# Kernel tuning notes

Hardware: AMD Instinct MI355X
Metric: run time of the kernel (lower is better)

## Reference

```python
import jax, jax.numpy as jnp
import numpy as np

B, S, D = 16, 2048, 128
SCALE = 1.0 / float(np.sqrt(D))  # scale = 1/sqrt(dim_K) per docstring


def setup_inputs() -> dict:
    key = jax.random.key(0)
    kq, kk, kv = jax.random.split(key, 3)
    Q = jax.random.normal(kq, (B, S, D), dtype=jnp.float32)
    K = jax.random.normal(kk, (B, S, D), dtype=jnp.float32)
    V = jax.random.normal(kv, (B, S, D), dtype=jnp.float32)
    return {"Q": Q, "K": K, "V": V}


def reference(Q, K, V):
    # attention = Q @ K^T * scale  -> [B, S, S]
    attn = jnp.einsum('bqd,bkd->bqk', Q, K) * SCALE
    attn = jax.nn.softmax(attn, axis=-1)
    # context = attn @ V -> [B, S, D]
    context = jnp.einsum('bqk,bkd->bqd', attn, V)
    return context
```

## Files before the change

kernel.cpp:

```cpp
#include <hip/hip_runtime.h>
#include <hip/hip_bf16.h>


#define NB 16
#define NS 2048
#define ND 128
#define KVB 32
#define NTT (NS / KVB)
#define IMG 16384
#define QSC (0.08838834764831845f * 1.4426950408889634f)

typedef __attribute__((ext_vector_type(8))) short bf16x8;
typedef __attribute__((ext_vector_type(4))) short short4v;
typedef __attribute__((ext_vector_type(16))) float f32x16;
typedef __attribute__((ext_vector_type(4))) int int4v;

__device__ __forceinline__ short f2bf(float f) {
    unsigned u = __builtin_bit_cast(unsigned, f);
    return (short)((u + 0x7fffu + ((u >> 16) & 1u)) >> 16);
}

#if __has_builtin(__builtin_amdgcn_exp2f)
#define EXP2F(x) __builtin_amdgcn_exp2f(x)
#else
#define EXP2F(x) __expf((x) * 0.6931471805599453f)
#endif

__device__ __forceinline__ void gll16(const void* g, void* l) {
    __builtin_amdgcn_global_load_lds(
        (const __attribute__((address_space(1))) uint32_t*)g,
        (__attribute__((address_space(3))) uint32_t*)l, 16, 0, 0);
}

__global__ __launch_bounds__(256, 2)
void prep_kv(const float* __restrict__ Kg, const float* __restrict__ Vg,
             uint8_t* __restrict__ ws) {
    __shared__ __align__(16) uint8_t img[2 * IMG];
    const int tid = threadIdx.x;
    const int t = blockIdx.x, b = blockIdx.y;
    const float* Kb = Kg + ((size_t)b * NS + (size_t)t * 64) * ND;
    const float* Vb = Vg + ((size_t)b * NS + (size_t)t * 64) * ND;
#pragma unroll
    for (int it = 0; it < 8; ++it) {
        int idx = it * 256 + tid;
        int r  = idx >> 5;
        int c4 = (idx & 31) << 2;
        int sub = (r >> 5) * (2 * 8192);
        int rr = r & 31;
        float4 kvv = *(const float4*)(Kb + (size_t)r * ND + c4);
        short4v ks = { f2bf(kvv.x), f2bf(kvv.y), f2bf(kvv.z), f2bf(kvv.w) };
        *(short4v*)&img[sub + rr * 256 + ((c4 * 2) ^ ((rr & 7) << 4))] = ks;
        float4 vv = *(const float4*)(Vb + (size_t)r * ND + c4);
        float vf[4] = { vv.x, vv.y, vv.z, vv.w };
#pragma unroll
        for (int di = 0; di < 4; ++di) {
            int d = c4 + di;
            *(short*)&img[sub + 8192 + d * 64 + ((rr * 2) ^ (((d >> 1) & 3) << 4))]
                = f2bf(vf[di]);
        }
    }
    __syncthreads();
    float4* dst = (float4*)(ws + (size_t)(b * (NTT / 2) + t) * (2 * IMG));
    const float4* srcl = (const float4*)img;
#pragma unroll
    for (int j = 0; j < 8; ++j)
        dst[j * 256 + tid] = srcl[j * 256 + tid];
}

__global__ __launch_bounds__(768, 3)
void sdpa_fwd(const float* __restrict__ Qg, const uint8_t* __restrict__ ws,
              float* __restrict__ Og) {
    __shared__ __align__(16) uint8_t kv[3][3][IMG];

    const int tid  = threadIdx.x;
    const int w    = tid >> 6;
    const int wq   = w & 3;
    const int wh   = w >> 2;
    const int lane = tid & 63;
    const int lr_  = lane & 31;
    const int hi   = lane >> 5;

    const int tlo  = (wh == 0) ? 0 : (22 + 21 * (wh - 1));
    const int tcnt = (wh == 0) ? 22 : 21;

    const int gid  = blockIdx.x;
    const int b    = (gid & 7) * 2 + ((gid >> 3) & 1);
    const int qblk = gid >> 4;
    const int q0w  = qblk * 128 + wq * 32;

    bf16x8 qf[8];
    {
        const float* qrow = Qg + ((size_t)b * NS + q0w + lr_) * ND;
#pragma unroll
        for (int dc = 0; dc < 8; ++dc) {
            const float4* p = (const float4*)(qrow + dc * 16 + hi * 8);
            float4 x0 = p[0], x1 = p[1];
            bf16x8 f;
            f[0] = f2bf(x0.x * QSC); f[1] = f2bf(x0.y * QSC);
            f[2] = f2bf(x0.z * QSC); f[3] = f2bf(x0.w * QSC);
            f[4] = f2bf(x1.x * QSC); f[5] = f2bf(x1.y * QSC);
            f[6] = f2bf(x1.z * QSC); f[7] = f2bf(x1.w * QSC);
            qf[dc] = f;
        }
    }

    f32x16 acc[4];
#pragma unroll
    for (int n = 0; n < 4; ++n)
#pragma unroll
        for (int r = 0; r < 16; ++r) acc[n][r] = 0.f;
    float m_run = -__builtin_inff();
    float l_run = 0.f;

    const uint8_t* wsb = ws + (size_t)b * NTT * IMG;

    const int kbase = lr_ * 256 + ((hi * 16) ^ ((lr_ & 7) << 4));
    const int vbase = 8192 + lr_ * 64 + ((hi * 16) ^ (((lr_ >> 1) & 3) << 4));

    auto st = [&](int tt, uint8_t* dst) {
        if (tt < tcnt) {
            const uint8_t* src = wsb + (size_t)(tlo + tt) * IMG
                                     + (size_t)(wq * 4096 + lane * 16);
            gll16(src,        dst);
            gll16(src + 1024, dst + 1024);
            gll16(src + 2048, dst + 2048);
            gll16(src + 3072, dst + 3072);
        }
    };

    auto qk = [&](int p, const uint8_t* img_, f32x16& sN) {
        if (p < tcnt) {
#pragma unroll
            for (int r = 0; r < 16; ++r) sN[r] = 0.f;
            __builtin_amdgcn_s_setprio(1);
#pragma unroll
            for (int dc = 0; dc < 8; ++dc) {
                bf16x8 k0 = *(const bf16x8*)(img_ + (kbase ^ (dc * 32)));
                sN = __builtin_amdgcn_mfma_f32_32x32x16_bf16(k0, qf[dc], sN, 0, 0, 0);
            }
            __builtin_amdgcn_s_setprio(0);
        }
    };

    auto sm = [&](int p, const uint8_t* img_, f32x16& sP) {
        if (p >= 0 && p < tcnt) {
            float tmax = -__builtin_inff();
#pragma unroll
            for (int r = 0; r < 16; ++r) tmax = fmaxf(tmax, sP[r]);
            float tm = fmaxf(tmax, __shfl_xor(tmax, 32));

            if (__any(tm > m_run + 8.0f)) {
                float m_new = fmaxf(m_run, tm);
                float alpha = EXP2F(m_run - m_new);
                m_run = m_new;
                l_run *= alpha;
#pragma unroll
                for (int r = 0; r < 16; ++r) {
                    float a = __shfl(alpha, (r & 3) + 8 * (r >> 2) + 4 * hi);
#pragma unroll
                    for (int n = 0; n < 4; ++n) acc[n][r] *= a;
                }
            }

            float ts = 0.f;
#pragma unroll
            for (int r = 0; r < 16; ++r) {
                sP[r] = EXP2F(sP[r] - m_run);
                ts += sP[r];
            }
            l_run += ts + __shfl_xor(ts, 32);

            int W[8];
#define PK(dst, x, y) asm("v_cvt_pk_bf16_f32 %0, %1, %2" : "=v"(dst) : "v"(x), "v"(y))
            PK(W[0], sP[0],  sP[1]);  PK(W[1], sP[2],  sP[3]);
            PK(W[2], sP[4],  sP[5]);  PK(W[3], sP[6],  sP[7]);
            PK(W[4], sP[8],  sP[9]);  PK(W[5], sP[10], sP[11]);
            PK(W[6], sP[12], sP[13]); PK(W[7], sP[14], sP[15]);
#undef PK
            bf16x8 pa[2];
#pragma unroll
            for (int g = 0; g < 2; ++g) {
                int W0 = W[g * 4 + 0], W1 = W[g * 4 + 1];
                int W2 = W[g * 4 + 2], W3 = W[g * 4 + 3];
                int X0 = __shfl_xor(W0, 32), X1 = __shfl_xor(W1, 32);
                int X2 = __shfl_xor(W2, 32), X3 = __shfl_xor(W3, 32);
                int4v A;
                A[0] = hi ? X2 : W0;
                A[1] = hi ? X3 : W1;
                A[2] = hi ? W2 : X0;
                A[3] = hi ? W3 : X1;
                pa[g] = __builtin_bit_cast(bf16x8, A);
            }

            __builtin_amdgcn_s_setprio(1);
#pragma unroll
            for (int n = 0; n < 4; ++n) {
#pragma unroll
                for (int kc = 0; kc < 2; ++kc) {
                    bf16x8 vf = *(const bf16x8*)(img_ + ((vbase ^ (kc * 32)) + n * 2048));
                    acc[n] = __builtin_amdgcn_mfma_f32_32x32x16_bf16(pa[kc], vf, acc[n], 0, 0, 0);
                }
            }
            __builtin_amdgcn_s_setprio(0);
        }
    };

    uint8_t* b0 = &kv[wh][0][0];
    uint8_t* b1 = &kv[wh][1][0];
    uint8_t* b2 = &kv[wh][2][0];
    const int so = wq * 4096;

    st(0, b0 + so);
    __syncthreads();

    f32x16 sA, sB;
    for (int i6 = 0; i6 < 4; ++i6) {
        const int base = i6 * 6;
        st(base + 1, b1 + so); qk(base + 0, b0, sA); sm(base - 1, b2, sB);
        __syncthreads();
        st(base + 2, b2 + so); qk(base + 1, b1, sB); sm(base + 0, b0, sA);
        __syncthreads();
        st(base + 3, b0 + so); qk(base + 2, b2, sA); sm(base + 1, b1, sB);
        __syncthreads();
        st(base + 4, b1 + so); qk(base + 3, b0, sB); sm(base + 2, b2, sA);
        __syncthreads();
        st(base + 5, b2 + so); qk(base + 4, b1, sA); sm(base + 3, b0, sB);
        __syncthreads();
        st(base + 6, b0 + so); qk(base + 5, b2, sB); sm(base + 4, b1, sA);
        __syncthreads();
    }

    float* scr = (float*)&kv[0][0][0];
    const int sbase = wq * 4224 + lane * 66;
#pragma unroll
    for (int rnd = 1; rnd <= 2; ++rnd) {
        __syncthreads();
        if (wh == rnd) {
#pragma unroll
            for (int n = 0; n < 4; ++n)
#pragma unroll
                for (int r = 0; r < 16; ++r) scr[sbase + n * 16 + r] = acc[n][r];
            scr[sbase + 64] = m_run;
            scr[sbase + 65] = l_run;
        }
        __syncthreads();
        if (wh == 0) {
            float m1 = scr[sbase + 64], l1 = scr[sbase + 65];
            float mm = fmaxf(m_run, m1);
            float a0 = EXP2F(m_run - mm), a1 = EXP2F(m1 - mm);
            l_run = l_run * a0 + l1 * a1;
            m_run = mm;
#pragma unroll
            for (int r = 0; r < 16; ++r) {
                int row = (r & 3) + 8 * (r >> 2) + 4 * hi;
                float f0 = __shfl(a0, row), f1 = __shfl(a1, row);
#pragma unroll
                for (int n = 0; n < 4; ++n)
                    acc[n][r] = acc[n][r] * f0 + scr[sbase + n * 16 + r] * f1;
            }
        }
    }

    if (wh == 0) {
        float* ob = Og + ((size_t)b * NS + q0w) * ND + lr_;
#pragma unroll
        for (int r = 0; r < 16; ++r) {
            int row = (r & 3) + 8 * (r >> 2) + 4 * hi;
            float li = 1.f / __shfl(l_run, row);
#pragma unroll
            for (int n = 0; n < 4; ++n)
                ob[(size_t)row * ND + n * 32] = acc[n][r] * li;
        }
    }
}

extern "C" void kernel_launch(void* const* d_in, const int* in_sizes, int n_in,
                              void* d_out, int out_size, void* d_ws, size_t ws_size,
                              hipStream_t stream) {
    const float* Q = (const float*)d_in[0];
    const float* K = (const float*)d_in[1];
    const float* V = (const float*)d_in[2];
    float* O = (float*)d_out;
    (void)in_sizes; (void)n_in; (void)out_size; (void)ws_size;
    uint8_t* ws = (uint8_t*)d_ws;
    prep_kv<<<dim3(NS / 64, NB), 256, 0, stream>>>(K, V, ws);
    sdpa_fwd<<<dim3(NB * NS / 128, 1), 768, 0, stream>>>(Q, ws, O);
}
```

Measured before the change: 67.81 us.

## Deepen K/V prefetch to two tiles ahead and merge QK with softmax per tile

The pipeline changes from a one-tile-ahead load, where QK^T of tile p overlapped with the softmax/PV of tile p-1, to a two-tiles-ahead prefetch with a fused per-tile compute (QK^T, softmax, PV in one step). Each phase waits only for the older global loads with a partial vmcnt wait before a raw s_barrier, instead of a full __syncthreads. The aim is to hide global-to-LDS latency better and cut barrier drain cost. In exchange it gives up the software overlap of MFMA from one tile with the exp work of the previous tile, and the hand-written waitcnt logic must match the number of loads issued in flight.

Result: faster. 65.23 us (-3.8%).

```diff
diff --git a/kernel.cpp b/kernel.cpp
--- a/kernel.cpp
+++ b/kernel.cpp
@@ -128,25 +128,22 @@
         }
     };
 
-    auto qk = [&](int p, const uint8_t* img_, f32x16& sN) {
+    auto comp = [&](int p, const uint8_t* img_) {
         if (p < tcnt) {
-#pragma unroll
-            for (int r = 0; r < 16; ++r) sN[r] = 0.f;
+            f32x16 s0;
+#pragma unroll
+            for (int r = 0; r < 16; ++r) s0[r] = 0.f;
             __builtin_amdgcn_s_setprio(1);
 #pragma unroll
             for (int dc = 0; dc < 8; ++dc) {
                 bf16x8 k0 = *(const bf16x8*)(img_ + (kbase ^ (dc * 32)));
-                sN = __builtin_amdgcn_mfma_f32_32x32x16_bf16(k0, qf[dc], sN, 0, 0, 0);
+                s0 = __builtin_amdgcn_mfma_f32_32x32x16_bf16(k0, qf[dc], s0, 0, 0, 0);
             }
             __builtin_amdgcn_s_setprio(0);
-        }
-    };
-
-    auto sm = [&](int p, const uint8_t* img_, f32x16& sP) {
-        if (p >= 0 && p < tcnt) {
+
             float tmax = -__builtin_inff();
 #pragma unroll
-            for (int r = 0; r < 16; ++r) tmax = fmaxf(tmax, sP[r]);
+            for (int r = 0; r < 16; ++r) tmax = fmaxf(tmax, s0[r]);
             float tm = fmaxf(tmax, __shfl_xor(tmax, 32));
 
             if (__any(tm > m_run + 8.0f)) {
@@ -165,17 +162,17 @@
             float ts = 0.f;
 #pragma unroll
             for (int r = 0; r < 16; ++r) {
-                sP[r] = EXP2F(sP[r] - m_run);
-                ts += sP[r];
+                s0[r] = EXP2F(s0[r] - m_run);
+                ts += s0[r];
             }
             l_run += ts + __shfl_xor(ts, 32);
 
             int W[8];
 #define PK(dst, x, y) asm("v_cvt_pk_bf16_f32 %0, %1, %2" : "=v"(dst) : "v"(x), "v"(y))
-            PK(W[0], sP[0],  sP[1]);  PK(W[1], sP[2],  sP[3]);
-            PK(W[2], sP[4],  sP[5]);  PK(W[3], sP[6],  sP[7]);
-            PK(W[4], sP[8],  sP[9]);  PK(W[5], sP[10], sP[11]);
-            PK(W[6], sP[12], sP[13]); PK(W[7], sP[14], sP[15]);
+            PK(W[0], s0[0],  s0[1]);  PK(W[1], s0[2],  s0[3]);
+            PK(W[2], s0[4],  s0[5]);  PK(W[3], s0[6],  s0[7]);
+            PK(W[4], s0[8],  s0[9]);  PK(W[5], s0[10], s0[11]);
+            PK(W[6], s0[12], s0[13]); PK(W[7], s0[14], s0[15]);
 #undef PK
             bf16x8 pa[2];
 #pragma unroll
@@ -210,25 +207,31 @@
     uint8_t* b2 = &kv[wh][2][0];
     const int so = wq * 4096;
 
+    auto phase = [&](int p, uint8_t* bS, const uint8_t* bC) {
+        st(p + 2, bS + so);
+        comp(p, bC);
+        if (p + 2 < tcnt) {
+            asm volatile("s_waitcnt vmcnt(4)" ::: "memory");
+        } else {
+            asm volatile("s_waitcnt vmcnt(0)" ::: "memory");
+        }
+        __builtin_amdgcn_s_barrier();
+        __builtin_amdgcn_sched_barrier(0);
+    };
+
     st(0, b0 + so);
-    __syncthreads();
-
-    f32x16 sA, sB;
-    for (int i6 = 0; i6 < 4; ++i6) {
-        const int base = i6 * 6;
-        st(base + 1, b1 + so); qk(base + 0, b0, sA); sm(base - 1, b2, sB);
-        __syncthreads();
-        st(base + 2, b2 + so); qk(base + 1, b1, sB); sm(base + 0, b0, sA);
-        __syncthreads();
-        st(base + 3, b0 + so); qk(base + 2, b2, sA); sm(base + 1, b1, sB);
-        __syncthreads();
-        st(base + 4, b1 + so); qk(base + 3, b0, sB); sm(base + 2, b2, sA);
-        __syncthreads();
-        st(base + 5, b2 + so); qk(base + 4, b1, sA); sm(base + 3, b0, sB);
-        __syncthreads();
-        st(base + 6, b0 + so); qk(base + 5, b2, sB); sm(base + 4, b1, sA);
-        __syncthreads();
-    }
+    st(1, b1 + so);
+    asm volatile("s_waitcnt vmcnt(4)" ::: "memory");
+    __builtin_amdgcn_s_barrier();
+    __builtin_amdgcn_sched_barrier(0);
+
+    for (int i3 = 0; i3 < 8; ++i3) {
+        const int base = i3 * 3;
+        phase(base + 0, b2, b0);
+        phase(base + 1, b0, b1);
+        phase(base + 2, b1, b2);
+    }
+    asm volatile("s_waitcnt vmcnt(0)" ::: "memory");
 
     float* scr = (float*)&kv[0][0][0];
     const int sbase = wq * 4224 + lane * 66;
```
